# Kernel tuning notes

Hardware: AMD Instinct MI355X
Metric: run time of the kernel (lower is better)

Reference implementation:

```python
import jax, jax.numpy as jnp
import numpy as np
from jax import lax

B, C, T = 512, 63, 250          # batch, EEG channels, timepoints
S = 10                           # number of subjects
E = 4                            # emb_size of CNN projection
HID, PROJ = 184, 1024            # hidden_dim (=4*46), embed_dim
EPS = 1e-5
DN = ('NCHW', 'OIHW', 'NCHW')


def setup_inputs() -> dict:
    key = jax.random.key(0)
    ks = jax.random.split(key, 16)
    p = {}
    p['x'] = jax.random.normal(ks[0], (B, C, T), dtype=jnp.float32)
    p['subjects'] = jax.random.randint(ks[1], (B,), 0, S, dtype=jnp.int32)
    # per-subject Linear(T, T): weight [S, T, T], bias [S, T]
    p['W_subj'] = jax.random.normal(ks[2], (S, T, T), dtype=jnp.float32) * 0.02
    p['b_subj'] = jnp.zeros((S, T), dtype=jnp.float32)
    # tsconv
    p['conv1_w'] = jax.random.normal(ks[3], (40, 1, 1, 5), dtype=jnp.float32) * 0.1
    p['conv1_b'] = jnp.zeros((40,), dtype=jnp.float32)
    p['bn1_g'] = jnp.ones((40,), dtype=jnp.float32)
    p['bn1_b'] = jnp.zeros((40,), dtype=jnp.float32)
    p['conv2_w'] = jax.random.normal(ks[4], (40, 40, C, 1), dtype=jnp.float32) * 0.02
    p['conv2_b'] = jnp.zeros((40,), dtype=jnp.float32)
    p['bn2_g'] = jnp.ones((40,), dtype=jnp.float32)
    p['bn2_b'] = jnp.zeros((40,), dtype=jnp.float32)
    # 1x1 projection conv to emb_size
    p['proj_w'] = jax.random.normal(ks[5], (E, 40, 1, 1), dtype=jnp.float32) * 0.1
    p['proj_b'] = jnp.zeros((E,), dtype=jnp.float32)
    # MLP projector
    p['fc1_w'] = jax.random.normal(ks[6], (PROJ, HID), dtype=jnp.float32) * 0.05
    p['fc1_b'] = jnp.zeros((PROJ,), dtype=jnp.float32)
    p['fc2_w'] = jax.random.normal(ks[7], (PROJ, PROJ), dtype=jnp.float32) * 0.02
    p['fc2_b'] = jnp.zeros((PROJ,), dtype=jnp.float32)
    p['ln_g'] = jnp.ones((PROJ,), dtype=jnp.float32)
    p['ln_b'] = jnp.zeros((PROJ,), dtype=jnp.float32)
    return p


def _bn(h, g, b):
    # BatchNorm2d with batch statistics over (N, H, W), NCHW layout
    mu = jnp.mean(h, axis=(0, 2, 3), keepdims=True)
    var = jnp.var(h, axis=(0, 2, 3), keepdims=True)
    return (h - mu) * lax.rsqrt(var + EPS) * g[None, :, None, None] + b[None, :, None, None]


def _avgpool_w(h, k, s):
    # average pool over last (W) dim, kernel k stride s
    summed = lax.reduce_window(h, 0.0, lax.add, (1, 1, 1, k), (1, 1, 1, s), 'VALID')
    return summed / k


def reference(x, subjects, W_subj, b_subj, conv1_w, conv1_b, bn1_g, bn1_b,
              conv2_w, conv2_b, bn2_g, bn2_b, proj_w, proj_b,
              fc1_w, fc1_b, fc2_w, fc2_b, ln_g, ln_b):
    # --- subject-conditioned linear dispatch (grouped GEMM via gather) ---
    Wg = W_subj[subjects]                      # [B, T, T]
    bg = b_subj[subjects]                      # [B, T]
    x_eeg = jnp.einsum('bct,bst->bcs', x, Wg) + bg[:, None, :]   # [B, C, T]

    # --- Spatio_Temporal_CNN ---
    h = x_eeg[:, None, :, :]                   # [B, 1, C, T]
    h = lax.conv_general_dilated(h, conv1_w, (1, 1), 'VALID', dimension_numbers=DN)
    h = h + conv1_b[None, :, None, None]       # [B, 40, C, 246]
    h = _avgpool_w(h, 17, 5)                   # [B, 40, C, 46]
    h = jax.nn.elu(_bn(h, bn1_g, bn1_b))
    h = lax.conv_general_dilated(h, conv2_w, (1, 1), 'VALID', dimension_numbers=DN)
    h = h + conv2_b[None, :, None, None]       # [B, 40, 1, 46]
    h = jax.nn.elu(_bn(h, bn2_g, bn2_b))       # dropout = identity (eval)
    h = lax.conv_general_dilated(h, proj_w, (1, 1), 'VALID', dimension_numbers=DN)
    h = h + proj_b[None, :, None, None]        # [B, E, 1, 46]
    # Rearrange 'b e h w -> b (h w) e' then flatten -> [B, 46*E] = [B, 184]
    z = jnp.transpose(h, (0, 2, 3, 1)).reshape(h.shape[0], -1)

    # --- MLP projector ---
    h1 = z @ fc1_w.T + fc1_b                   # [B, 1024]
    r = jax.nn.gelu(h1, approximate=False) @ fc2_w.T + fc2_b
    h2 = h1 + r                                # ResidualAdd (dropout = identity)
    mu = jnp.mean(h2, axis=-1, keepdims=True)
    var = jnp.var(h2, axis=-1, keepdims=True)
    return (h2 - mu) * lax.rsqrt(var + EPS) * ln_g + ln_b
```

## Files before the change

### kernel.cpp

```cpp
#include <hip/hip_runtime.h>
#include <hip/hip_bf16.h>

#define K2 2520
#define PROJ 1024
#define HID 184
#define N1F (512.f*63.f*46.f)
#define N2F (512.f*46.f)

typedef float f32x4 __attribute__((ext_vector_type(4)));
typedef short bf16x8 __attribute__((ext_vector_type(8)));
typedef unsigned short u16;
typedef unsigned short ushort8 __attribute__((ext_vector_type(8)));

__device__ __forceinline__ u16 f2bf(float f) {
    unsigned u = __builtin_bit_cast(unsigned, f);
    return (u16)((u + 0x7FFFu + ((u >> 16) & 1u)) >> 16);
}
__device__ __forceinline__ float bf2f(u16 h) {
    unsigned u = ((unsigned)h) << 16;
    return __builtin_bit_cast(float, u);
}

__global__ void kX(const float* __restrict__ W, const float* __restrict__ w2,
                   const float* __restrict__ fw1, const float* __restrict__ fw2,
                   u16* __restrict__ Wbf, u16* __restrict__ Wbf2,
                   u16* __restrict__ fwbf1, u16* __restrict__ fwbf2, float* stats) {
    int bid = blockIdx.x, tid = threadIdx.x;
    if (bid == 0 && tid < 320) stats[tid] = 0.f;
    if (bid < 2560) {
        int i = bid*256 + tid;
        int sj = i >> 16, s_ = (i >> 8) & 255, t_ = i & 255;
        float v = (s_ < 250 && t_ < 250) ? W[(size_t)sj*62500 + s_*250 + t_] : 0.f;
        Wbf[i] = f2bf(v);
    } else if (bid < 3034) {
        int i = (bid-2560)*256 + tid;
        int n = i / 2528, k = i - n*2528;
        float v = 0.f;
        if (n < 40 && k < K2) { int c = k/40, o = k - c*40; v = w2[n*K2 + o*63 + c]; }
        Wbf2[i] = f2bf(v);
    } else if (bid < 3802) {
        int i = (bid-3034)*256 + tid;
        int n = i/192, k = i - n*192;
        fwbf1[i] = f2bf(k < HID ? fw1[n*HID + k] : 0.f);
    } else {
        int i = (bid-3802)*256 + tid;
        fwbf2[i] = f2bf(fw2[i]);
    }
}

#define XS(c,s) xs[(c)*258 + (s)]
__global__ __launch_bounds__(256) void kAB(const float* __restrict__ x,
                                           const int* __restrict__ subj,
                                           const u16* __restrict__ Wbf,
                                           const float* __restrict__ bsub,
                                           const float* __restrict__ w1,
                                           const float* __restrict__ b1,
                                           u16* __restrict__ pooled,
                                           float* __restrict__ stats) {
    __shared__ float xs[32 * 258];
    __shared__ float effs[40 * 22];
    __shared__ float biasL[256];
    __shared__ float sS[6][40], sQ[6][40];
    int b = blockIdx.x, ch = blockIdx.y;
    int sj = subj[b];
    int tid = threadIdx.x;
    int wv = tid >> 6, lane = tid & 63, row = lane & 15, kg = lane >> 4;

    biasL[tid] = (tid < 250) ? bsub[sj*250 + tid] : 0.f;
    for (int i = tid; i < 840; i += 256) {
        int o = i / 21, j = i - o * 21;
        float e = 0.f;
        #pragma unroll
        for (int k = 0; k < 5; ++k) { int u = j - k; if (u >= 0 && u <= 16) e += w1[o*5+k]; }
        effs[o*22 + j] = e * (1.f / 17.f);
    }

    int cgrp = wv & 1, nfh = wv >> 1;
    int cglob = ch*32 + cgrp*16 + row;
    const float* xr = x + ((size_t)b*63 + (cglob < 63 ? cglob : 62))*250;
    const u16* Wb = Wbf + (size_t)sj*65536;
    f32x4 acc[8];
    #pragma unroll
    for (int i = 0; i < 8; ++i) acc[i] = (f32x4){0.f,0.f,0.f,0.f};
    #pragma unroll
    for (int ks = 0; ks < 8; ++ks) {
        int tb = ks*32 + kg*8;
        float av[8];
        if (ks < 7) {
            #pragma unroll
            for (int j = 0; j < 8; j += 2) { float2 v = *(const float2*)&xr[tb+j]; av[j]=v.x; av[j+1]=v.y; }
        } else {
            #pragma unroll
            for (int j = 0; j < 8; ++j) av[j] = 0.f;
            if (kg < 3) {
                #pragma unroll
                for (int j = 0; j < 8; j += 2) { float2 v = *(const float2*)&xr[tb+j]; av[j]=v.x; av[j+1]=v.y; }
            } else {
                float2 v = *(const float2*)&xr[248]; av[0]=v.x; av[1]=v.y;
            }
        }
        bf16x8 af;
        #pragma unroll
        for (int j = 0; j < 8; ++j) af[j] = (short)f2bf(av[j]);
        #pragma unroll
        for (int nf2 = 0; nf2 < 8; ++nf2) {
            int nf = nfh*8 + nf2;
            bf16x8 bv = *(const bf16x8*)(Wb + (size_t)(nf*16 + row)*256 + tb);
            acc[nf2] = __builtin_amdgcn_mfma_f32_16x16x32_bf16(af, bv, acc[nf2], 0, 0, 0);
        }
    }
    __syncthreads();
    int cw = cgrp*16 + kg*4;
    #pragma unroll
    for (int nf2 = 0; nf2 < 8; ++nf2) {
        int s = (nfh*8 + nf2)*16 + row;
        float bias = biasL[s];
        #pragma unroll
        for (int r = 0; r < 4; ++r) XS(cw + r, s) = acc[nf2][r] + bias;
    }
    __syncthreads();

    int climit = ch ? 31 : 32;
    if (tid < 240) {
        int o = tid % 40, cg = tid / 40;
        float eff[21];
        #pragma unroll
        for (int j = 0; j < 21; ++j) eff[j] = effs[o*22 + j];
        float bo = b1[o];
        float ssum = 0.f, ssq = 0.f;
        u16* prow = pooled + (size_t)b * 46 * K2;
        for (int c2 = cg; c2 < climit; c2 += 6) {
            float win[21];
            #pragma unroll
            for (int j = 0; j < 21; ++j) win[j] = XS(c2, j);
            int kidx = (ch*32 + c2)*40 + o;
            #pragma unroll
            for (int w = 0; w < 46; ++w) {
                float a = bo;
                #pragma unroll
                for (int j = 0; j < 21; ++j) a = fmaf(win[j], eff[j], a);
                prow[(size_t)w*K2 + kidx] = f2bf(a);
                ssum += a; ssq = fmaf(a, a, ssq);
                if (w < 45) {
                    #pragma unroll
                    for (int j2 = 0; j2 < 16; ++j2) win[j2] = win[j2+5];
                    #pragma unroll
                    for (int j2 = 16; j2 < 21; ++j2) win[j2] = XS(c2, 5*w + 5 + j2);
                }
            }
        }
        sS[cg][o] = ssum; sQ[cg][o] = ssq;
    }
    __syncthreads();
    if (tid < 40) {
        float s = 0.f, q = 0.f;
        #pragma unroll
        for (int g = 0; g < 6; ++g) { s += sS[g][tid]; q += sQ[g][tid]; }
        atomicAdd(&stats[tid], s);
        atomicAdd(&stats[40 + tid], q);
    }
}

__global__ void kC(float* stats, const float* __restrict__ g1, const float* __restrict__ bb1) {
    int t = threadIdx.x;
    if (t < 40) {
        float mean = stats[t] / N1F;
        float var  = stats[40 + t] / N1F - mean * mean;
        float sc   = g1[t] * rsqrtf(var + 1e-5f);
        stats[80 + t]  = sc;
        stats[120 + t] = bb1[t] - mean * sc;
    }
}

__global__ __launch_bounds__(256) void kD(const u16* __restrict__ pooled,
                                          const u16* __restrict__ Wbf2,
                                          const float* __restrict__ b2,
                                          const float* __restrict__ stats,
                                          float* __restrict__ out2,
                                          float* __restrict__ statw) {
    __shared__ float2 scsh[40];
    __shared__ float mrg[2][64][12];
    __shared__ float redS[2][48], redQ[2][48];
    int tid = threadIdx.x;
    if (tid < 40) scsh[tid] = make_float2(stats[80 + tid], stats[120 + tid]);
    __syncthreads();
    int wv = tid >> 6, lane = tid & 63, row = lane & 15, kg = lane >> 4;
    int rowgrp = wv >> 1, khalf = wv & 1;
    int mbase = blockIdx.x*32 + rowgrp*16;
    const u16* pr = pooled + (size_t)(mbase + row) * K2;
    f32x4 acc[3];
    #pragma unroll
    for (int i = 0; i < 3; ++i) acc[i] = (f32x4){0.f,0.f,0.f,0.f};

    int ksBeg = khalf ? 39 : 0, ksEnd = khalf ? 79 : 39;
    for (int ks = ksBeg; ks < ksEnd; ++ks) {
        int kbase = ks*32 + kg*8;
        ushort8 cur = *(const ushort8*)&pr[kbase];
        bf16x8 bv0 = *(const bf16x8*)(Wbf2 + (size_t)(row     )*2528 + kbase);
        bf16x8 bv1 = *(const bf16x8*)(Wbf2 + (size_t)(16 + row)*2528 + kbase);
        bf16x8 bv2 = *(const bf16x8*)(Wbf2 + (size_t)(32 + row)*2528 + kbase);
        bf16x8 af;
        bool valid = (ks < 78) | (kg < 3);
        if (valid) {
            #pragma unroll
            for (int j = 0; j < 8; ++j) {
                int k = kbase + j;
                int u = (k * 1639) >> 16;
                int o = k - u*40;
                float2 sshf = scsh[o];
                float a = fmaf(bf2f(cur[j]), sshf.x, sshf.y);
                float e = a > 0.f ? a : __expf(a) - 1.f;
                af[j] = (short)f2bf(e);
            }
        } else {
            #pragma unroll
            for (int j = 0; j < 8; ++j) af[j] = 0;
        }
        acc[0] = __builtin_amdgcn_mfma_f32_16x16x32_bf16(af, bv0, acc[0], 0, 0, 0);
        acc[1] = __builtin_amdgcn_mfma_f32_16x16x32_bf16(af, bv1, acc[1], 0, 0, 0);
        acc[2] = __builtin_amdgcn_mfma_f32_16x16x32_bf16(af, bv2, acc[2], 0, 0, 0);
    }

    if (khalf) {
        #pragma unroll
        for (int nf = 0; nf < 3; ++nf)
            #pragma unroll
            for (int r = 0; r < 4; ++r) mrg[rowgrp][lane][nf*4 + r] = acc[nf][r];
    }
    __syncthreads();
    if (!khalf) {
        float sN[3] = {0.f,0.f,0.f}, qN[3] = {0.f,0.f,0.f};
        #pragma unroll
        for (int nf = 0; nf < 3; ++nf) {
            int n = nf*16 + row;
            #pragma unroll
            for (int r = 0; r < 4; ++r) acc[nf][r] += mrg[rowgrp][lane][nf*4 + r];
            if (n < 40) {
                float bias = b2[n];
                #pragma unroll
                for (int r = 0; r < 4; ++r) {
                    float v = acc[nf][r] + bias;
                    out2[(size_t)(mbase + kg*4 + r)*40 + n] = v;
                    sN[nf] += v; qN[nf] += v*v;
                }
            }
        }
        #pragma unroll
        for (int nf = 0; nf < 3; ++nf) {
            float s = sN[nf], q = qN[nf];
            s += __shfl_xor(s, 16); q += __shfl_xor(q, 16);
            s += __shfl_xor(s, 32); q += __shfl_xor(q, 32);
            if (kg == 0) { redS[rowgrp][nf*16 + row] = s; redQ[rowgrp][nf*16 + row] = q; }
        }
    }
    __syncthreads();
    if (tid < 40) {
        atomicAdd(&statw[160 + tid], redS[0][tid] + redS[1][tid]);
        atomicAdd(&statw[200 + tid], redQ[0][tid] + redQ[1][tid]);
    }
}

__global__ void kE2(float* stats, const float* __restrict__ g2, const float* __restrict__ bb2) {
    int t = threadIdx.x;
    if (t < 40) {
        float mean = stats[160 + t] / N2F;
        float var  = stats[200 + t] / N2F - mean * mean;
        float s    = g2[t] * rsqrtf(var + 1e-5f);
        stats[240 + t] = s;
        stats[280 + t] = bb2[t] - mean * s;
    }
}

__global__ void kF(const float* __restrict__ out2, const float* __restrict__ stats,
                   const float* __restrict__ pw, const float* __restrict__ pb,
                   u16* __restrict__ zbf) {
    int b = blockIdx.x, t = threadIdx.x;
    __shared__ float sc[40], sh[40], pws[160];
    __shared__ float o2[1840];
    if (t < 40) { sc[t] = stats[240 + t]; sh[t] = stats[280 + t]; }
    if (t < 160) pws[t] = pw[t];
    for (int i = t; i < 1840; i += 256) o2[i] = out2[(size_t)b*1840 + i];
    __syncthreads();
    if (t < 192) {
        float accv = 0.f;
        if (t < HID) {
            int w = t >> 2, e = t & 3;
            accv = pb[e];
            for (int o = 0; o < 40; ++o) {
                float a = o2[w*40 + o];
                float act = a * sc[o] + sh[o];
                act = act > 0.f ? act : __expf(act) - 1.f;
                accv = fmaf(act, pws[e*40 + o], accv);
            }
        }
        zbf[(size_t)b*192 + t] = f2bf(accv);
    }
}

__global__ __launch_bounds__(256) void kG1(const u16* __restrict__ zbf, const u16* __restrict__ fwbf1,
                                           const float* __restrict__ fb,
                                           float* __restrict__ h1, u16* __restrict__ gbf) {
    int n0 = blockIdx.x * 64, m0 = blockIdx.y * 16;
    int tid = threadIdx.x, wv = tid >> 6, lane = tid & 63, row = lane & 15, kg = lane >> 4;
    const u16* zr = zbf + (size_t)(m0 + row) * 192;
    const u16* wr = fwbf1 + (size_t)(n0 + wv*16 + row) * 192;
    f32x4 acc = (f32x4){0.f,0.f,0.f,0.f};
    #pragma unroll
    for (int ks = 0; ks < 6; ++ks) {
        bf16x8 av = *(const bf16x8*)(zr + ks*32 + kg*8);
        bf16x8 bv = *(const bf16x8*)(wr + ks*32 + kg*8);
        acc = __builtin_amdgcn_mfma_f32_16x16x32_bf16(av, bv, acc, 0, 0, 0);
    }
    int n = n0 + wv*16 + row;
    float bias = fb[n];
    #pragma unroll
    for (int r = 0; r < 4; ++r) {
        int m = m0 + kg*4 + r;
        float v = acc[r] + bias;
        h1[(size_t)m*PROJ + n] = v;
        float ge = 0.5f * v * (1.f + erff(v * 0.70710678118f));
        gbf[(size_t)m*PROJ + n] = f2bf(ge);
    }
}

__global__ __launch_bounds__(256) void kG2(const u16* __restrict__ gbf, const u16* __restrict__ fwbf,
                                           const float* __restrict__ fb, const float* __restrict__ h1,
                                           float* __restrict__ h2) {
    int n0 = blockIdx.x * 32, m0 = blockIdx.y * 64;
    int tid = threadIdx.x;
    int wv = tid >> 6, lane = tid & 63, row = lane & 15, kg = lane >> 4;
    const u16* gr = gbf + (size_t)(m0 + wv*16 + row) * PROJ;
    f32x4 acc[2];
    #pragma unroll
    for (int i = 0; i < 2; ++i) acc[i] = (f32x4){0.f,0.f,0.f,0.f};
    for (int ks = 0; ks < 32; ++ks) {
        int kbase = ks*32 + kg*8;
        bf16x8 av  = *(const bf16x8*)(gr + kbase);
        bf16x8 bv0 = *(const bf16x8*)(fwbf + (size_t)(n0      + row)*PROJ + kbase);
        bf16x8 bv1 = *(const bf16x8*)(fwbf + (size_t)(n0 + 16 + row)*PROJ + kbase);
        acc[0] = __builtin_amdgcn_mfma_f32_16x16x32_bf16(av, bv0, acc[0], 0, 0, 0);
        acc[1] = __builtin_amdgcn_mfma_f32_16x16x32_bf16(av, bv1, acc[1], 0, 0, 0);
    }
    int m = m0 + wv*16 + kg*4;
    #pragma unroll
    for (int nf = 0; nf < 2; ++nf) {
        int n = n0 + nf*16 + row;
        float bias = fb[n];
        #pragma unroll
        for (int r = 0; r < 4; ++r)
            h2[(size_t)(m + r)*PROJ + n] = acc[nf][r] + bias + h1[(size_t)(m + r)*PROJ + n];
    }
}

__global__ __launch_bounds__(256) void kG3(const float* __restrict__ h2, const float* __restrict__ lg,
                                           const float* __restrict__ lb, float* __restrict__ out) {
    int b = blockIdx.x, tid = threadIdx.x;
    float4 v = *(const float4*)&h2[(size_t)b*PROJ + tid*4];
    float s = v.x + v.y + v.z + v.w;
    float q = v.x*v.x + v.y*v.y + v.z*v.z + v.w*v.w;
    __shared__ float ps[4], pq[4], mb[2];
    int wave = tid >> 6, lane = tid & 63;
    #pragma unroll
    for (int d = 32; d >= 1; d >>= 1) { s += __shfl_down(s, d); q += __shfl_down(q, d); }
    if (lane == 0) { ps[wave] = s; pq[wave] = q; }
    __syncthreads();
    if (tid == 0) {
        float S = ps[0]+ps[1]+ps[2]+ps[3], Q = pq[0]+pq[1]+pq[2]+pq[3];
        float mean = S / 1024.f, var = Q / 1024.f - mean*mean;
        mb[0] = mean; mb[1] = rsqrtf(var + 1e-5f);
    }
    __syncthreads();
    float mean = mb[0], inv = mb[1];
    float4 g4 = *(const float4*)&lg[tid*4];
    float4 b4 = *(const float4*)&lb[tid*4];
    float4 o4;
    o4.x = (v.x - mean)*inv*g4.x + b4.x;
    o4.y = (v.y - mean)*inv*g4.y + b4.y;
    o4.z = (v.z - mean)*inv*g4.z + b4.z;
    o4.w = (v.w - mean)*inv*g4.w + b4.w;
    *(float4*)&out[(size_t)b*PROJ + tid*4] = o4;
}

extern "C" void kernel_launch(void* const* d_in, const int* in_sizes, int n_in,
                              void* d_out, int out_size, void* d_ws, size_t ws_size,
                              hipStream_t stream) {
    const float* x       = (const float*)d_in[0];
    const int*   subjects= (const int*)  d_in[1];
    const float* W_subj  = (const float*)d_in[2];
    const float* b_subj  = (const float*)d_in[3];
    const float* conv1_w = (const float*)d_in[4];
    const float* conv1_b = (const float*)d_in[5];
    const float* bn1_g   = (const float*)d_in[6];
    const float* bn1_b   = (const float*)d_in[7];
    const float* conv2_w = (const float*)d_in[8];
    const float* conv2_b = (const float*)d_in[9];
    const float* bn2_g   = (const float*)d_in[10];
    const float* bn2_b   = (const float*)d_in[11];
    const float* proj_w  = (const float*)d_in[12];
    const float* proj_b  = (const float*)d_in[13];
    const float* fc1_w   = (const float*)d_in[14];
    const float* fc1_b   = (const float*)d_in[15];
    const float* fc2_w   = (const float*)d_in[16];
    const float* fc2_b   = (const float*)d_in[17];
    const float* ln_g    = (const float*)d_in[18];
    const float* ln_b    = (const float*)d_in[19];
    float* out = (float*)d_out;

    char* ws = (char*)d_ws;
    u16*   pooled = (u16*)  ws;
    float* out2   = (float*)(ws + 118702144);
    u16*   zbf    = (u16*)  (ws + 122470464);
    float* h1     = (float*)(ws + 122667072);
    float* h2     = (float*)(ws + 124764224);
    u16*   gbf    = (u16*)  (ws + 126861376);
    float* stats  = (float*)(ws + 127909952);
    u16*   Wbf    = (u16*)  (ws + 127914048);
    u16*   Wbf2   = (u16*)  (ws + 129224768);
    u16*   fwbf2  = (u16*)  (ws + 129467456);
    u16*   fwbf1  = (u16*)  (ws + 131564608);

    kX  <<<7898, 256, 0, stream>>>(W_subj, conv2_w, fc1_w, fc2_w, Wbf, Wbf2, fwbf1, fwbf2, stats);
    kAB <<<dim3(512, 2), 256, 0, stream>>>(x, subjects, Wbf, b_subj, conv1_w, conv1_b, pooled, stats);
    kC  <<<1, 64, 0, stream>>>(stats, bn1_g, bn1_b);
    kD  <<<736, 256, 0, stream>>>(pooled, Wbf2, conv2_b, stats, out2, stats);
    kE2 <<<1, 64, 0, stream>>>(stats, bn2_g, bn2_b);
    kF  <<<512, 256, 0, stream>>>(out2, stats, proj_w, proj_b, zbf);
    kG1 <<<dim3(16, 32), 256, 0, stream>>>(zbf, fwbf1, fc1_b, h1, gbf);
    kG2 <<<dim3(32, 8), 256, 0, stream>>>(gbf, fwbf2, fc2_b, h1, h2);
    kG3 <<<512, 256, 0, stream>>>(h2, ln_g, ln_b, out);
    (void)in_sizes; (void)n_in; (void)out_size; (void)ws_size;
}
```

Baseline: 291.4 us.

## Remap kAB pooling work to channel-by-output-group threads and fold BN finalize kernels

```diff
diff --git a/kernel.cpp b/kernel.cpp
--- a/kernel.cpp
+++ b/kernel.cpp
@@ -60,7 +60,7 @@
     __shared__ float xs[32 * 258];
     __shared__ float effs[40 * 22];
     __shared__ float biasL[256];
-    __shared__ float sS[6][40], sQ[6][40];
+    __shared__ float sS[4][8][5], sQ[4][8][5];
     int b = blockIdx.x, ch = blockIdx.y;
     int sj = subj[b];
     int tid = threadIdx.x;
@@ -120,61 +120,69 @@
     }
     __syncthreads();
 
-    int climit = ch ? 31 : 32;
-    if (tid < 240) {
-        int o = tid % 40, cg = tid / 40;
-        float eff[21];
-        #pragma unroll
-        for (int j = 0; j < 21; ++j) eff[j] = effs[o*22 + j];
-        float bo = b1[o];
-        float ssum = 0.f, ssq = 0.f;
-        u16* prow = pooled + (size_t)b * 46 * K2;
-        for (int c2 = cg; c2 < climit; c2 += 6) {
-            float win[21];
-            #pragma unroll
-            for (int j = 0; j < 21; ++j) win[j] = XS(c2, j);
-            int kidx = (ch*32 + c2)*40 + o;
-            #pragma unroll
-            for (int w = 0; w < 46; ++w) {
-                float a = bo;
+    int c2 = tid >> 3, og = tid & 7;
+    bool rowvalid = (ch == 0) || (c2 < 31);
+    float eff[5][21];
+    float bo[5];
+    #pragma unroll
+    for (int i = 0; i < 5; ++i) {
+        int o = og*5 + i;
+        bo[i] = b1[o];
+        #pragma unroll
+        for (int j = 0; j < 21; ++j) eff[i][j] = effs[o*22 + j];
+    }
+    float ssum[5] = {0.f,0.f,0.f,0.f,0.f}, ssq[5] = {0.f,0.f,0.f,0.f,0.f};
+    if (rowvalid) {
+        float win[21];
+        #pragma unroll
+        for (int j = 0; j < 21; ++j) win[j] = XS(c2, j);
+        u16* prow = pooled + (size_t)b*46*K2 + (ch*32 + c2)*40 + og*5;
+        for (int w = 0; w < 46; ++w) {
+            float a[5];
+            #pragma unroll
+            for (int i = 0; i < 5; ++i) {
+                float s = bo[i];
                 #pragma unroll
-                for (int j = 0; j < 21; ++j) a = fmaf(win[j], eff[j], a);
-                prow[(size_t)w*K2 + kidx] = f2bf(a);
-                ssum += a; ssq = fmaf(a, a, ssq);
-                if (w < 45) {
-                    #pragma unroll
-                    for (int j2 = 0; j2 < 16; ++j2) win[j2] = win[j2+5];
-                    #pragma unroll
-                    for (int j2 = 16; j2 < 21; ++j2) win[j2] = XS(c2, 5*w + 5 + j2);
-                }
-            }
-        }
-        sS[cg][o] = ssum; sQ[cg][o] = ssq;
+                for (int j = 0; j < 21; ++j) s = fmaf(win[j], eff[i][j], s);
+                a[i] = s;
+            }
+            #pragma unroll
+            for (int i = 0; i < 5; ++i) {
+                prow[(size_t)w*K2 + i] = f2bf(a[i]);
+                ssum[i] += a[i];
+                ssq[i] = fmaf(a[i], a[i], ssq[i]);
+            }
+            if (w < 45) {
+                #pragma unroll
+                for (int j2 = 0; j2 < 16; ++j2) win[j2] = win[j2+5];
+                #pragma unroll
+                for (int j2 = 16; j2 < 21; ++j2) win[j2] = XS(c2, 5*w + 5 + j2);
+            }
+        }
+    }
+    #pragma unroll
+    for (int i = 0; i < 5; ++i) {
+        float s = ssum[i], q = ssq[i];
+        s += __shfl_xor(s, 8);  q += __shfl_xor(q, 8);
+        s += __shfl_xor(s, 16); q += __shfl_xor(q, 16);
+        s += __shfl_xor(s, 32); q += __shfl_xor(q, 32);
+        if ((lane >> 3) == 0) { sS[wv][lane][i] = s; sQ[wv][lane][i] = q; }
     }
     __syncthreads();
     if (tid < 40) {
-        float s = 0.f, q = 0.f;
-        #pragma unroll
-        for (int g = 0; g < 6; ++g) { s += sS[g][tid]; q += sQ[g][tid]; }
+        int og2 = tid / 5, i2 = tid - og2*5;
+        float s = sS[0][og2][i2] + sS[1][og2][i2] + sS[2][og2][i2] + sS[3][og2][i2];
+        float q = sQ[0][og2][i2] + sQ[1][og2][i2] + sQ[2][og2][i2] + sQ[3][og2][i2];
         atomicAdd(&stats[tid], s);
         atomicAdd(&stats[40 + tid], q);
-    }
-}
-
-__global__ void kC(float* stats, const float* __restrict__ g1, const float* __restrict__ bb1) {
-    int t = threadIdx.x;
-    if (t < 40) {
-        float mean = stats[t] / N1F;
-        float var  = stats[40 + t] / N1F - mean * mean;
-        float sc   = g1[t] * rsqrtf(var + 1e-5f);
-        stats[80 + t]  = sc;
-        stats[120 + t] = bb1[t] - mean * sc;
     }
 }
 
 __global__ __launch_bounds__(256) void kD(const u16* __restrict__ pooled,
                                           const u16* __restrict__ Wbf2,
                                           const float* __restrict__ b2,
+                                          const float* __restrict__ g1,
+                                          const float* __restrict__ bb1,
                                           const float* __restrict__ stats,
                                           float* __restrict__ out2,
                                           float* __restrict__ statw) {
@@ -182,7 +190,12 @@
     __shared__ float mrg[2][64][12];
     __shared__ float redS[2][48], redQ[2][48];
     int tid = threadIdx.x;
-    if (tid < 40) scsh[tid] = make_float2(stats[80 + tid], stats[120 + tid]);
+    if (tid < 40) {
+        float mean = stats[tid] / N1F;
+        float var  = stats[40 + tid] / N1F - mean * mean;
+        float sc   = g1[tid] * rsqrtf(var + 1e-5f);
+        scsh[tid] = make_float2(sc, bb1[tid] - mean * sc);
+    }
     __syncthreads();
     int wv = tid >> 6, lane = tid & 63, row = lane & 15, kg = lane >> 4;
     int rowgrp = wv >> 1, khalf = wv & 1;
@@ -260,24 +273,20 @@
     }
 }
 
-__global__ void kE2(float* stats, const float* __restrict__ g2, const float* __restrict__ bb2) {
-    int t = threadIdx.x;
-    if (t < 40) {
-        float mean = stats[160 + t] / N2F;
-        float var  = stats[200 + t] / N2F - mean * mean;
-        float s    = g2[t] * rsqrtf(var + 1e-5f);
-        stats[240 + t] = s;
-        stats[280 + t] = bb2[t] - mean * s;
-    }
-}
-
 __global__ void kF(const float* __restrict__ out2, const float* __restrict__ stats,
+                   const float* __restrict__ g2, const float* __restrict__ bb2,
                    const float* __restrict__ pw, const float* __restrict__ pb,
                    u16* __restrict__ zbf) {
     int b = blockIdx.x, t = threadIdx.x;
     __shared__ float sc[40], sh[40], pws[160];
     __shared__ float o2[1840];
-    if (t < 40) { sc[t] = stats[240 + t]; sh[t] = stats[280 + t]; }
+    if (t < 40) {
+        float mean = stats[160 + t] / N2F;
+        float var  = stats[200 + t] / N2F - mean * mean;
+        float s    = g2[t] * rsqrtf(var + 1e-5f);
+        sc[t] = s;
+        sh[t] = bb2[t] - mean * s;
+    }
     if (t < 160) pws[t] = pw[t];
     for (int i = t; i < 1840; i += 256) o2[i] = out2[(size_t)b*1840 + i];
     __syncthreads();
@@ -421,10 +430,8 @@
 
     kX  <<<7898, 256, 0, stream>>>(W_subj, conv2_w, fc1_w, fc2_w, Wbf, Wbf2, fwbf1, fwbf2, stats);
     kAB <<<dim3(512, 2), 256, 0, stream>>>(x, subjects, Wbf, b_subj, conv1_w, conv1_b, pooled, stats);
-    kC  <<<1, 64, 0, stream>>>(stats, bn1_g, bn1_b);
-    kD  <<<736, 256, 0, stream>>>(pooled, Wbf2, conv2_b, stats, out2, stats);
-    kE2 <<<1, 64, 0, stream>>>(stats, bn2_g, bn2_b);
-    kF  <<<512, 256, 0, stream>>>(out2, stats, proj_w, proj_b, zbf);
+    kD  <<<736, 256, 0, stream>>>(pooled, Wbf2, conv2_b, bn1_g, bn1_b, stats, out2, stats);
+    kF  <<<512, 256, 0, stream>>>(out2, stats, bn2_g, bn2_b, proj_w, proj_b, zbf);
     kG1 <<<dim3(16, 32), 256, 0, stream>>>(zbf, fwbf1, fc1_b, h1, gbf);
     kG2 <<<dim3(32, 8), 256, 0, stream>>>(gbf, fwbf2, fc2_b, h1, h2);
     kG3 <<<512, 256, 0, stream>>>(h2, ln_g, ln_b, out);
```

After: 309.4 us. +6.2%, slower.
